# Kernel optimization log

Hardware: AMD Instinct MI355X
Metric: run time of the kernel (lower is better)

Reference implementation:

```python
import jax, jax.numpy as jnp
import numpy as np

EPS = 1e-5
NUM_HEADS = 4
KEY_DIM = 16
HEAD_DIM = 16


def qconv(x, w, b=None, stride=1, pad=0, groups=1):
    """Quaternion conv via Hamilton product. x:[B,C,4,H,W], w:[4,Cout,Cin/g,kh,kw]."""
    def cc(a, ww):
        return jax.lax.conv_general_dilated(
            a, ww, (stride, stride), [(pad, pad), (pad, pad)],
            feature_group_count=groups,
            dimension_numbers=('NCHW', 'OIHW', 'NCHW'))
    xr, xi, xj, xk = x[:, :, 0], x[:, :, 1], x[:, :, 2], x[:, :, 3]
    wr, wi, wj, wk = w[0], w[1], w[2], w[3]
    yr = cc(xr, wr) - cc(xi, wi) - cc(xj, wj) - cc(xk, wk)
    yi = cc(xr, wi) + cc(xi, wr) + cc(xj, wk) - cc(xk, wj)
    yj = cc(xr, wj) - cc(xi, wk) + cc(xj, wr) + cc(xk, wi)
    yk = cc(xr, wk) + cc(xi, wj) - cc(xj, wi) + cc(xk, wr)
    y = jnp.stack([yr, yi, yj, yk], axis=2)  # [B,Cout,4,H,W]
    if b is not None:
        y = y + b[None, :, :, None, None]
    return y


def iqbn(x, g, b):
    """Independent quaternion batch norm: per (channel, component) over (B,H,W)."""
    mean = x.mean(axis=(0, 3, 4), keepdims=True)
    var = x.var(axis=(0, 3, 4), keepdims=True)
    xhat = (x - mean) * jax.lax.rsqrt(var + EPS)
    return g[None, :, :, None, None] * xhat + b[None, :, :, None, None]


def qattention(x, qkv_w, qkv_b, proj_w, proj_b, pe_w, pe_b, ng, nb):
    B, C, Q, H, W = x.shape
    N = H * W
    qkv = qconv(x, qkv_w, qkv_b)                       # [B,h,4,H,W]
    qkv = qkv.reshape(B, NUM_HEADS, 2 * KEY_DIM + HEAD_DIM, Q, N)
    q = qkv[:, :, :KEY_DIM]                             # [B,nh,kd,4,N]
    k = qkv[:, :, KEY_DIM:2 * KEY_DIM]                  # [B,nh,kd,4,N]
    v = qkv[:, :, 2 * KEY_DIM:]                         # [B,nh,hd,4,N]
    scale = KEY_DIM ** (-0.5)
    attn = jnp.einsum('bhdqn,bhdqm->bhqnm', q, k) * scale   # [B,nh,4,N,N]
    attn = jax.nn.softmax(attn, axis=-1)
    o = jnp.einsum('bhqnm,bhdqm->bhdqn', attn, v)       # [B,nh,hd,4,N]
    o = o.reshape(B, C, Q, H, W)
    pe = qconv(o, pe_w, pe_b, stride=1, pad=1, groups=C // 4)
    o = o + pe
    o = qconv(o, proj_w, proj_b)
    return iqbn(o, ng, nb)


def setup_inputs() -> dict:
    key = jax.random.key(0)
    ks = jax.random.split(key, 16)
    c1, c2, c = 128, 128, 64
    h = c + 2 * NUM_HEADS * KEY_DIM  # 192
    s = 0.05
    x = jax.random.normal(ks[0], (4, c1, 4, 32, 32), dtype=jnp.float32)
    return {
        'x': x,
        'cv1_w': jax.random.normal(ks[1], (4, 2 * c, c1, 1, 1), jnp.float32) * s,
        'bn1_g': jnp.ones((2 * c, 4), jnp.float32),
        'bn1_b': jnp.zeros((2 * c, 4), jnp.float32),
        'qkv_w': jax.random.normal(ks[2], (4, h, c, 1, 1), jnp.float32) * s,
        'qkv_b': jnp.zeros((h, 4), jnp.float32),
        'proj_w': jax.random.normal(ks[3], (4, c, c, 1, 1), jnp.float32) * s,
        'proj_b': jnp.zeros((c, 4), jnp.float32),
        'pe_w': jax.random.normal(ks[4], (4, c, 4, 3, 3), jnp.float32) * s,  # groups=c//4=16
        'pe_b': jnp.zeros((c, 4), jnp.float32),
        'attn_norm_g': jnp.ones((c, 4), jnp.float32),
        'attn_norm_b': jnp.zeros((c, 4), jnp.float32),
        'ffn1_w': jax.random.normal(ks[5], (4, 2 * c, c, 1, 1), jnp.float32) * s,
        'ffn_bn1_g': jnp.ones((2 * c, 4), jnp.float32),
        'ffn_bn1_b': jnp.zeros((2 * c, 4), jnp.float32),
        'ffn2_w': jax.random.normal(ks[6], (4, c, 2 * c, 1, 1), jnp.float32) * s,
        'ffn_bn2_g': jnp.ones((c, 4), jnp.float32),
        'ffn_bn2_b': jnp.zeros((c, 4), jnp.float32),
        'cv2_w': jax.random.normal(ks[7], (4, c2, 2 * c, 1, 1), jnp.float32) * s,
        'bn2_g': jnp.ones((c2, 4), jnp.float32),
        'bn2_b': jnp.zeros((c2, 4), jnp.float32),
    }


def reference(x, cv1_w, bn1_g, bn1_b, qkv_w, qkv_b, proj_w, proj_b, pe_w, pe_b,
              attn_norm_g, attn_norm_b, ffn1_w, ffn_bn1_g, ffn_bn1_b,
              ffn2_w, ffn_bn2_g, ffn_bn2_b, cv2_w, bn2_g, bn2_b):
    h = jax.nn.relu(iqbn(qconv(x, cv1_w), bn1_g, bn1_b))  # [B,2c,4,H,W]
    c = h.shape[1] // 2
    a, b = h[:, :c], h[:, c:]
    a = qattention(a, qkv_w, qkv_b, proj_w, proj_b, pe_w, pe_b, attn_norm_g, attn_norm_b)
    a = jax.nn.relu(iqbn(qconv(a, ffn1_w), ffn_bn1_g, ffn_bn1_b))
    a = iqbn(qconv(a, ffn2_w), ffn_bn2_g, ffn_bn2_b)
    out = jnp.concatenate([a, b], axis=1)
    out = jax.nn.relu(iqbn(qconv(out, cv2_w), bn2_g, bn2_b))
    return out
```

## Files before the change

kernel.cpp:

```cpp
#include <hip/hip_runtime.h>

#define N_PIX 1024

typedef __attribute__((ext_vector_type(8))) short bf16x8;
typedef __attribute__((ext_vector_type(4))) float f32x4;

__device__ inline ushort f2bf(float f) {
    union { float f; unsigned u; } v; v.f = f;
    unsigned u = v.u;
    return (ushort)((u + 0x7FFF + ((u >> 16) & 1)) >> 16);
}
__device__ inline float bf2f(ushort h) {
    union { unsigned u; float f; } v; v.u = ((unsigned)h) << 16; return v.f;
}

__global__ __launch_bounds__(256) void wexpand_kernel(
    const float* __restrict__ w, ushort* __restrict__ wx, int Cout, int Cin)
{
    int idx = blockIdx.x * 256 + threadIdx.x;
    int K = 4 * Cin;
    if (idx >= 4 * Cout * K) return;
    int m = idx / K, k = idx - m * K;
    int co = m >> 2, c = m & 3, ci = k >> 2, cp = k & 3;
    const int   CT[4][4] = {{0,1,2,3},{1,0,3,2},{2,3,0,1},{3,2,1,0}};
    const float ST[4][4] = {{1.f,-1.f,-1.f,-1.f},{1.f,1.f,1.f,-1.f},
                            {1.f,-1.f,1.f,1.f},{1.f,1.f,-1.f,1.f}};
    float val = ST[c][cp] * w[(size_t)CT[c][cp] * Cout * Cin + (size_t)co * Cin + ci];
    wx[idx] = f2bf(val);
}

__global__ __launch_bounds__(256) void pack_kernel(
    const float* __restrict__ src, int sbs, ushort* __restrict__ xp, int K)
{
    __shared__ float t[32][257];
    const int k0 = blockIdx.x * 32;
    const int P0 = blockIdx.y * 256;
    const int b = P0 >> 10, p0 = P0 & 1023;
    const float* s = src + (size_t)b * sbs + (size_t)k0 * N_PIX + p0;
#pragma unroll
    for (int i = 0; i < 32; i++)
        t[i][threadIdx.x] = s[i * N_PIX + threadIdx.x];
    __syncthreads();
#pragma unroll
    for (int j = 0; j < 32; j++) {
        int flat = j * 256 + threadIdx.x;
        int kk = flat & 31, p = flat >> 5;
        xp[(size_t)(P0 + p) * K + k0 + kk] = f2bf(t[kk][p]);
    }
}

__global__ __launch_bounds__(256) void qgemm_kernel(
    const ushort* __restrict__ xp,
    const ushort* __restrict__ wx,
    const float* __restrict__ bias,
    float* __restrict__ y, int ybs,
    int M, int K)
{
    __shared__ ushort As[64 * 32];
    __shared__ ushort Bs[128 * 32];
    const int tid = threadIdx.x;
    const int m0 = blockIdx.x * 64;
    const int P0 = blockIdx.y * 128;
    const int b  = P0 >> 10;
    const int p0 = P0 & 1023;
    const int w  = tid >> 6;
    const int l  = tid & 63;
    const int wm = w >> 1, wn = w & 1;

    const f32x4 z = {0.f, 0.f, 0.f, 0.f};
    f32x4 acc[2][4];
#pragma unroll
    for (int mi = 0; mi < 2; mi++)
#pragma unroll
        for (int ni = 0; ni < 4; ni++) acc[mi][ni] = z;

    const int am  = tid >> 2, akb = tid & 3;
    const int lkb = l >> 4,   lr  = l & 15;

    for (int k0 = 0; k0 < K; k0 += 32) {
        __syncthreads();
        *(int4*)&As[((akb * 64) + am) * 8] =
            *(const int4*)&wx[(size_t)(m0 + am) * K + k0 + akb * 8];
#pragma unroll
        for (int it = 0; it < 2; it++) {
            int n = it * 64 + (tid >> 2);
            *(int4*)&Bs[((akb * 128) + n) * 8] =
                *(const int4*)&xp[(size_t)(P0 + n) * K + k0 + akb * 8];
        }
        __syncthreads();

        bf16x8 af[2], bf[4];
#pragma unroll
        for (int mi = 0; mi < 2; mi++)
            af[mi] = *(const bf16x8*)&As[((lkb * 64) + wm * 32 + mi * 16 + lr) * 8];
#pragma unroll
        for (int ni = 0; ni < 4; ni++)
            bf[ni] = *(const bf16x8*)&Bs[((lkb * 128) + wn * 64 + ni * 16 + lr) * 8];
#pragma unroll
        for (int mi = 0; mi < 2; mi++)
#pragma unroll
            for (int ni = 0; ni < 4; ni++)
                acc[mi][ni] = __builtin_amdgcn_mfma_f32_16x16x32_bf16(
                    af[mi], bf[ni], acc[mi][ni], 0, 0, 0);
    }

    float* yb = y + (size_t)b * ybs;
#pragma unroll
    for (int mi = 0; mi < 2; mi++) {
        int mrow = m0 + wm * 32 + mi * 16 + lkb * 4;
#pragma unroll
        for (int ni = 0; ni < 4; ni++) {
            int col = p0 + wn * 64 + ni * 16 + lr;
#pragma unroll
            for (int r = 0; r < 4; r++) {
                float v = acc[mi][ni][r];
                if (bias) v += bias[mrow + r];
                yb[(size_t)(mrow + r) * N_PIX + col] = v;
            }
        }
    }
}

__global__ __launch_bounds__(256) void iqbn_stats_kernel(
    const float* __restrict__ x, int xbs, float* __restrict__ stats)
{
    const int cq = blockIdx.x;
    float s = 0.f, s2 = 0.f;
#pragma unroll
    for (int b = 0; b < 4; b++) {
        const float* xp = x + (size_t)b * xbs + (size_t)cq * N_PIX;
        for (int p = threadIdx.x; p < N_PIX; p += 256) {
            float v = xp[p];
            s += v; s2 += v * v;
        }
    }
#pragma unroll
    for (int o = 32; o > 0; o >>= 1) {
        s  += __shfl_down(s, o);
        s2 += __shfl_down(s2, o);
    }
    __shared__ float red[8];
    int wid = threadIdx.x >> 6, lane = threadIdx.x & 63;
    if (lane == 0) { red[wid * 2] = s; red[wid * 2 + 1] = s2; }
    __syncthreads();
    if (threadIdx.x == 0) {
        s = 0.f; s2 = 0.f;
#pragma unroll
        for (int i = 0; i < 4; i++) { s += red[2 * i]; s2 += red[2 * i + 1]; }
        const float inv = 1.0f / 4096.0f;
        float mean = s * inv;
        float var  = s2 * inv - mean * mean;
        stats[cq * 2]     = mean;
        stats[cq * 2 + 1] = rsqrtf(var + 1e-5f);
    }
}

__global__ __launch_bounds__(256) void iqbn_apply_kernel(
    const float* __restrict__ x, int xbs,
    float* __restrict__ y, int ybs,
    const float* __restrict__ stats,
    const float* __restrict__ g, const float* __restrict__ bta,
    int C4, int relu)
{
    int cq = blockIdx.x % C4;
    int b  = blockIdx.x / C4;
    float mean = stats[cq * 2], rstd = stats[cq * 2 + 1];
    float ga = g[cq] * rstd;
    float bb = bta[cq] - mean * ga;
    const float4* xp = (const float4*)(x + (size_t)b * xbs + (size_t)cq * N_PIX);
    float4*       yp = (float4*)(y + (size_t)b * ybs + (size_t)cq * N_PIX);
    float4 v = xp[threadIdx.x];
    v.x = v.x * ga + bb; v.y = v.y * ga + bb; v.z = v.z * ga + bb; v.w = v.w * ga + bb;
    if (relu) {
        v.x = fmaxf(v.x, 0.f); v.y = fmaxf(v.y, 0.f);
        v.z = fmaxf(v.z, 0.f); v.w = fmaxf(v.w, 0.f);
    }
    yp[threadIdx.x] = v;
}

__global__ __launch_bounds__(256) void qattn_kernel(
    const float* __restrict__ qkv, float* __restrict__ o)
{
    __shared__ __attribute__((aligned(16))) char smem[24576];
    const int tid = threadIdx.x;
    const int grp = blockIdx.x;
    const int qc = grp & 3, hd = (grp >> 2) & 3, b = grp >> 4;
    const int n0 = blockIdx.y << 7;
    const int w = tid >> 6, lid = tid & 63;
    const int col = lid & 15, g = lid >> 4;
    const int swz = (col & 7) << 4;

    const float* gq = qkv + ((size_t)(b * 192 + hd * 48) * 4 + qc) * N_PIX;

    bf16x8 qf[2];
#pragma unroll
    for (int ns = 0; ns < 2; ns++) {
        int n = n0 + w * 32 + ns * 16 + col;
        const float* qg = gq + (size_t)((g & 1) * 8) * 4096 + n;
        union { bf16x8 v; ushort u[8]; } qq;
#pragma unroll
        for (int j = 0; j < 8; j++) {
            float qv = qg[(size_t)j * 4096] * 0.25f;
            ushort h = f2bf(qv);
            qq.u[j] = (g >= 2) ? f2bf(qv - bf2f(h)) : h;
        }
        qf[ns] = qq.v;
    }

    const f32x4 z = {0.f, 0.f, 0.f, 0.f};
    f32x4 O[2] = {z, z};
    float M[2] = {-1e30f, -1e30f}, L[2] = {0.f, 0.f};

    const int ml = tid & 63;
    const int d4 = (tid >> 6) << 2;

    for (int t = 0; t < 16; t++) {
        const int m0 = t << 6;
        __syncthreads();
        {
            const float* kg = gq + (size_t)(16 + d4) * 4096 + m0 + ml;
            const float* vg = gq + (size_t)(32 + d4) * 4096 + m0 + ml;
            float kv[4], vv[4];
#pragma unroll
            for (int i = 0; i < 4; i++) {
                kv[i] = kg[(size_t)i * 4096];
                vv[i] = vg[(size_t)i * 4096];
            }
            ushort kh[4], kl[4];
#pragma unroll
            for (int i = 0; i < 4; i++) {
                kh[i] = f2bf(kv[i]);
                kl[i] = f2bf(kv[i] - bf2f(kh[i]));
            }
            int sw = (ml & 7) << 4;
            int kbh = (ml * 64 + d4 * 2) ^ sw;
            int kbl = (ml * 64 + 32 + d4 * 2) ^ sw;
            *(uint2*)(smem + kbh) =
                make_uint2((uint)kh[0] | ((uint)kh[1] << 16), (uint)kh[2] | ((uint)kh[3] << 16));
            *(uint2*)(smem + kbl) =
                make_uint2((uint)kl[0] | ((uint)kl[1] << 16), (uint)kl[2] | ((uint)kl[3] << 16));
#pragma unroll
            for (int i = 0; i < 4; i++) {
                int d = d4 + i;
                ushort vh = f2bf(vv[i]);
                ushort vl = f2bf(vv[i] - bf2f(vh));
                int vb = (d * 128 + ml * 2) ^ ((d & 7) << 4);
                *(ushort*)(smem + 4096 + vb) = vh;
                *(ushort*)(smem + 6144 + vb) = vl;
            }
        }
        __syncthreads();

        f32x4 s[2][4];
#pragma unroll
        for (int ms = 0; ms < 4; ms++) {
            int rowb = (ms * 16 + col) * 64;
            bf16x8 a1 = *(const bf16x8*)(smem + ((rowb + g * 16) ^ swz));
            bf16x8 a2 = *(const bf16x8*)(smem + ((rowb + ((g ^ 2) * 16)) ^ swz));
#pragma unroll
            for (int ns = 0; ns < 2; ns++) {
                f32x4 c = __builtin_amdgcn_mfma_f32_16x16x32_bf16(a1, qf[ns], z, 0, 0, 0);
                s[ns][ms] = __builtin_amdgcn_mfma_f32_16x16x32_bf16(a2, qf[ns], c, 0, 0, 0);
            }
        }

#pragma unroll
        for (int ns = 0; ns < 2; ns++) {
            float tmax = s[ns][0][0];
#pragma unroll
            for (int ms = 0; ms < 4; ms++)
#pragma unroll
                for (int r = 0; r < 4; r++) tmax = fmaxf(tmax, s[ns][ms][r]);
            tmax = fmaxf(tmax, __shfl_xor(tmax, 16));
            tmax = fmaxf(tmax, __shfl_xor(tmax, 32));
            float Mn = fmaxf(M[ns], tmax);
            float rs = __expf(M[ns] - Mn);
            M[ns] = Mn;
            float psum = 0.f;
#pragma unroll
            for (int ms = 0; ms < 4; ms++) {
                f32x4 e;
#pragma unroll
                for (int r = 0; r < 4; r++) {
                    e[r] = __expf(s[ns][ms][r] - Mn);
                    psum += e[r];
                }
                s[ns][ms] = e;
            }
            psum += __shfl_xor(psum, 16);
            psum += __shfl_xor(psum, 32);
            L[ns] = L[ns] * rs + psum;
#pragma unroll
            for (int r = 0; r < 4; r++)
                O[ns][r] *= __shfl(rs, g * 4 + r);
            int nl = ns * 16 + col;
#pragma unroll
            for (int ms = 0; ms < 4; ms++) {
                uint plo = (uint)f2bf(s[ns][ms][0]) | ((uint)f2bf(s[ns][ms][1]) << 16);
                uint phi = (uint)f2bf(s[ns][ms][2]) | ((uint)f2bf(s[ns][ms][3]) << 16);
                int pb = (8192 + w * 4096 + nl * 128 + ms * 32 + g * 8) ^ swz;
                *(uint2*)(smem + pb) = make_uint2(plo, phi);
            }
        }
        __builtin_amdgcn_sched_barrier(0);

#pragma unroll
        for (int s2 = 0; s2 < 2; s2++) {
            int mb = s2 * 64 + g * 16;
            int vb = (col * 128 + mb) ^ swz;
            bf16x8 bvh = *(const bf16x8*)(smem + 4096 + vb);
            bf16x8 bvl = *(const bf16x8*)(smem + 6144 + vb);
#pragma unroll
            for (int ns = 0; ns < 2; ns++) {
                int nl = ns * 16 + col;
                bf16x8 ap = *(const bf16x8*)(smem + ((8192 + w * 4096 + nl * 128 + mb) ^ swz));
                O[ns] = __builtin_amdgcn_mfma_f32_16x16x32_bf16(ap, bvh, O[ns], 0, 0, 0);
                O[ns] = __builtin_amdgcn_mfma_f32_16x16x32_bf16(ap, bvl, O[ns], 0, 0, 0);
            }
        }
    }

#pragma unroll
    for (int ns = 0; ns < 2; ns++) {
        float invL = 1.f / L[ns];
#pragma unroll
        for (int r = 0; r < 4; r++)
            O[ns][r] *= __shfl(invL, g * 4 + r);
    }
    __syncthreads();
#pragma unroll
    for (int ns = 0; ns < 2; ns++) {
        int nloc = w * 32 + ns * 16 + g * 4;
        int ob = (8192 + col * 512 + nloc * 4) ^ swz;
        *(f32x4*)(smem + ob) = O[ns];
    }
    __syncthreads();
    {
        int d = tid >> 4, nb = (tid & 15) << 3;
        int b0 = (8192 + d * 512 + nb * 4) ^ ((d & 7) << 4);
        int b1 = (8192 + d * 512 + nb * 4 + 16) ^ ((d & 7) << 4);
        float4 o0 = *(const float4*)(smem + b0);
        float4 o1 = *(const float4*)(smem + b1);
        float* op = o + ((size_t)(b * 64 + hd * 16 + d) * 4 + qc) * N_PIX + n0 + nb;
        *(float4*)op = o0;
        *(float4*)(op + 4) = o1;
    }
}

__global__ __launch_bounds__(256) void pe_conv_kernel(
    const float* __restrict__ x,
    const float* __restrict__ w,
    const float* __restrict__ bias,
    float* __restrict__ y)
{
    const int bid = blockIdx.x;
    const int pt = bid & 3, co = (bid >> 2) & 63, b = bid >> 8;
    const int p = (pt << 8) + threadIdx.x;
    const int hh = p >> 5, ww = p & 31;
    const int g4 = (co >> 2) << 2;

    float a0 = bias[co * 4 + 0], a1 = bias[co * 4 + 1];
    float a2 = bias[co * 4 + 2], a3 = bias[co * 4 + 3];
    const float* xb = x + (size_t)b * 64 * 4096;
    const float* wb = w + co * 36;

#pragma unroll
    for (int dy = 0; dy < 3; dy++) {
        int yy = hh + dy - 1;
        if ((unsigned)yy >= 32u) continue;
#pragma unroll
        for (int dx = 0; dx < 3; dx++) {
            int xx = ww + dx - 1;
            if ((unsigned)xx >= 32u) continue;
            int sp = yy * 32 + xx;
#pragma unroll
            for (int cl = 0; cl < 4; cl++) {
                const float* xp = xb + (size_t)(g4 + cl) * 4096 + sp;
                float xr = xp[0], xi = xp[1024], xj = xp[2048], xk = xp[3072];
                const float* wp = wb + cl * 9 + dy * 3 + dx;
                float wr = wp[0], wi = wp[2304], wj2 = wp[4608], wk = wp[6912];
                a0 += xr * wr - xi * wi  - xj * wj2 - xk * wk;
                a1 += xr * wi + xi * wr  + xj * wk  - xk * wj2;
                a2 += xr * wj2 - xi * wk + xj * wr  + xk * wi;
                a3 += xr * wk + xi * wj2 - xj * wi  + xk * wr;
            }
        }
    }
    size_t ob = (size_t)b * 64 * 4096 + (size_t)co * 4096 + p;
    y[ob]        = x[ob]        + a0;
    y[ob + 1024] = x[ob + 1024] + a1;
    y[ob + 2048] = x[ob + 2048] + a2;
    y[ob + 3072] = x[ob + 3072] + a3;
}

extern "C" void kernel_launch(void* const* d_in, const int* in_sizes, int n_in,
                              void* d_out, int out_size, void* d_ws, size_t ws_size,
                              hipStream_t stream)
{
    const float* x      = (const float*)d_in[0];
    const float* cv1_w  = (const float*)d_in[1];
    const float* bn1_g  = (const float*)d_in[2];
    const float* bn1_b  = (const float*)d_in[3];
    const float* qkv_w  = (const float*)d_in[4];
    const float* qkv_b  = (const float*)d_in[5];
    const float* proj_w = (const float*)d_in[6];
    const float* proj_b = (const float*)d_in[7];
    const float* pe_w   = (const float*)d_in[8];
    const float* pe_b   = (const float*)d_in[9];
    const float* ang    = (const float*)d_in[10];
    const float* anb    = (const float*)d_in[11];
    const float* ffn1_w = (const float*)d_in[12];
    const float* fbn1_g = (const float*)d_in[13];
    const float* fbn1_b = (const float*)d_in[14];
    const float* ffn2_w = (const float*)d_in[15];
    const float* fbn2_g = (const float*)d_in[16];
    const float* fbn2_b = (const float*)d_in[17];
    const float* cv2_w  = (const float*)d_in[18];
    const float* bn2_g  = (const float*)d_in[19];
    const float* bn2_b  = (const float*)d_in[20];
    float* out = (float*)d_out;

    float* ws    = (float*)d_ws;
    float* hbuf  = ws;
    float* qkvb  = ws + 2097152;
    float* bufA  = ws + 5242880;
    float* bufD  = ws + 6291456;
    float* stats = ws + 8388608;
    ushort* Xp   = (ushort*)(ws + 8389632);
    ushort* Wx   = (ushort*)(ws + 9438208);
    float* bufB  = qkvb;
    float* bufC  = qkvb + 1048576;
    float* cv2o  = qkvb;

    const int S128 = 128 * 4096, S192 = 192 * 4096, S64 = 64 * 4096;

    wexpand_kernel<<<1024, 256, 0, stream>>>(cv1_w, Wx, 128, 128);
    pack_kernel<<<dim3(16, 16), 256, 0, stream>>>(x, S128, Xp, 512);
    qgemm_kernel<<<dim3(8, 32), 256, 0, stream>>>(Xp, Wx, nullptr, hbuf, S128, 512, 512);
    iqbn_stats_kernel<<<512, 256, 0, stream>>>(hbuf, S128, stats);
    iqbn_apply_kernel<<<2048, 256, 0, stream>>>(hbuf, S128, hbuf, S128, stats, bn1_g, bn1_b, 512, 1);

    wexpand_kernel<<<768, 256, 0, stream>>>(qkv_w, Wx, 192, 64);
    pack_kernel<<<dim3(8, 16), 256, 0, stream>>>(hbuf, S128, Xp, 256);
    qgemm_kernel<<<dim3(12, 32), 256, 0, stream>>>(Xp, Wx, qkv_b, qkvb, S192, 768, 256);

    qattn_kernel<<<dim3(64, 8), 256, 0, stream>>>(qkvb, bufA);

    pe_conv_kernel<<<1024, 256, 0, stream>>>(bufA, pe_w, pe_b, bufB);

    wexpand_kernel<<<256, 256, 0, stream>>>(proj_w, Wx, 64, 64);
    pack_kernel<<<dim3(8, 16), 256, 0, stream>>>(bufB, S64, Xp, 256);
    qgemm_kernel<<<dim3(4, 32), 256, 0, stream>>>(Xp, Wx, proj_b, bufC, S64, 256, 256);
    iqbn_stats_kernel<<<256, 256, 0, stream>>>(bufC, S64, stats);
    iqbn_apply_kernel<<<1024, 256, 0, stream>>>(bufC, S64, bufC, S64, stats, ang, anb, 256, 0);

    wexpand_kernel<<<512, 256, 0, stream>>>(ffn1_w, Wx, 128, 64);
    pack_kernel<<<dim3(8, 16), 256, 0, stream>>>(bufC, S64, Xp, 256);
    qgemm_kernel<<<dim3(8, 32), 256, 0, stream>>>(Xp, Wx, nullptr, bufD, S128, 512, 256);
    iqbn_stats_kernel<<<512, 256, 0, stream>>>(bufD, S128, stats);
    iqbn_apply_kernel<<<2048, 256, 0, stream>>>(bufD, S128, bufD, S128, stats, fbn1_g, fbn1_b, 512, 1);

    wexpand_kernel<<<512, 256, 0, stream>>>(ffn2_w, Wx, 64, 128);
    pack_kernel<<<dim3(16, 16), 256, 0, stream>>>(bufD, S128, Xp, 512);
    qgemm_kernel<<<dim3(4, 32), 256, 0, stream>>>(Xp, Wx, nullptr, bufA, S64, 256, 512);
    iqbn_stats_kernel<<<256, 256, 0, stream>>>(bufA, S64, stats);
    iqbn_apply_kernel<<<1024, 256, 0, stream>>>(bufA, S64, hbuf, S128, stats, fbn2_g, fbn2_b, 256, 0);

    wexpand_kernel<<<1024, 256, 0, stream>>>(cv2_w, Wx, 128, 128);
    pack_kernel<<<dim3(16, 16), 256, 0, stream>>>(hbuf, S128, Xp, 512);
    qgemm_kernel<<<dim3(8, 32), 256, 0, stream>>>(Xp, Wx, nullptr, cv2o, S128, 512, 512);
    iqbn_stats_kernel<<<512, 256, 0, stream>>>(cv2o, S128, stats);
    iqbn_apply_kernel<<<2048, 256, 0, stream>>>(cv2o, S128, out, S128, stats, bn2_g, bn2_b, 512, 1);
}
```

Measured before the change: 307.2 us.

## Fuse BN stats into GEMM epilogue and BN apply into bf16 packing

The new GEMM kernel uses a 64x64 tile with double-buffered LDS and register prefetch, and accumulates per-channel sum and sum-of-squares via shuffle reductions and atomics in its epilogue. This removes the separate stats pass. BN apply, ReLU and transpose-to-bf16 packing are fused into one kernel that writes straight into the next GEMM's packed input, including the concat split into the cv2 input buffer. This drops several full-tensor read/write passes and launches. In exchange it relies on float atomics, so stat accumulation order is nondeterministic, and variance is computed from raw sums.

After: 364.6 us. +18.7%, slower.

```diff
diff --git a/kernel.cpp b/kernel.cpp
--- a/kernel.cpp
+++ b/kernel.cpp
@@ -12,6 +12,12 @@
 }
 __device__ inline float bf2f(ushort h) {
     union { unsigned u; float f; } v; v.u = ((unsigned)h) << 16; return v.f;
+}
+
+__global__ __launch_bounds__(256) void zero_kernel(float* __restrict__ p, int n)
+{
+    int i = blockIdx.x * 256 + threadIdx.x;
+    if (i < n) p[i] = 0.f;
 }
 
 __global__ __launch_bounds__(256) void wexpand_kernel(
@@ -49,126 +55,60 @@
     }
 }
 
-__global__ __launch_bounds__(256) void qgemm_kernel(
-    const ushort* __restrict__ xp,
-    const ushort* __restrict__ wx,
-    const float* __restrict__ bias,
-    float* __restrict__ y, int ybs,
-    int M, int K)
-{
-    __shared__ ushort As[64 * 32];
-    __shared__ ushort Bs[128 * 32];
-    const int tid = threadIdx.x;
-    const int m0 = blockIdx.x * 64;
-    const int P0 = blockIdx.y * 128;
-    const int b  = P0 >> 10;
-    const int p0 = P0 & 1023;
-    const int w  = tid >> 6;
-    const int l  = tid & 63;
-    const int wm = w >> 1, wn = w & 1;
-
-    const f32x4 z = {0.f, 0.f, 0.f, 0.f};
-    f32x4 acc[2][4];
-#pragma unroll
-    for (int mi = 0; mi < 2; mi++)
-#pragma unroll
-        for (int ni = 0; ni < 4; ni++) acc[mi][ni] = z;
-
-    const int am  = tid >> 2, akb = tid & 3;
-    const int lkb = l >> 4,   lr  = l & 15;
-
-    for (int k0 = 0; k0 < K; k0 += 32) {
-        __syncthreads();
-        *(int4*)&As[((akb * 64) + am) * 8] =
-            *(const int4*)&wx[(size_t)(m0 + am) * K + k0 + akb * 8];
-#pragma unroll
-        for (int it = 0; it < 2; it++) {
-            int n = it * 64 + (tid >> 2);
-            *(int4*)&Bs[((akb * 128) + n) * 8] =
-                *(const int4*)&xp[(size_t)(P0 + n) * K + k0 + akb * 8];
-        }
-        __syncthreads();
-
-        bf16x8 af[2], bf[4];
-#pragma unroll
-        for (int mi = 0; mi < 2; mi++)
-            af[mi] = *(const bf16x8*)&As[((lkb * 64) + wm * 32 + mi * 16 + lr) * 8];
-#pragma unroll
-        for (int ni = 0; ni < 4; ni++)
-            bf[ni] = *(const bf16x8*)&Bs[((lkb * 128) + wn * 64 + ni * 16 + lr) * 8];
-#pragma unroll
-        for (int mi = 0; mi < 2; mi++)
-#pragma unroll
-            for (int ni = 0; ni < 4; ni++)
-                acc[mi][ni] = __builtin_amdgcn_mfma_f32_16x16x32_bf16(
-                    af[mi], bf[ni], acc[mi][ni], 0, 0, 0);
-    }
-
-    float* yb = y + (size_t)b * ybs;
-#pragma unroll
-    for (int mi = 0; mi < 2; mi++) {
-        int mrow = m0 + wm * 32 + mi * 16 + lkb * 4;
-#pragma unroll
-        for (int ni = 0; ni < 4; ni++) {
-            int col = p0 + wn * 64 + ni * 16 + lr;
-#pragma unroll
-            for (int r = 0; r < 4; r++) {
-                float v = acc[mi][ni][r];
-                if (bias) v += bias[mrow + r];
-                yb[(size_t)(mrow + r) * N_PIX + col] = v;
-            }
-        }
-    }
-}
-
-__global__ __launch_bounds__(256) void iqbn_stats_kernel(
-    const float* __restrict__ x, int xbs, float* __restrict__ stats)
-{
-    const int cq = blockIdx.x;
-    float s = 0.f, s2 = 0.f;
-#pragma unroll
-    for (int b = 0; b < 4; b++) {
-        const float* xp = x + (size_t)b * xbs + (size_t)cq * N_PIX;
-        for (int p = threadIdx.x; p < N_PIX; p += 256) {
-            float v = xp[p];
-            s += v; s2 += v * v;
-        }
-    }
-#pragma unroll
-    for (int o = 32; o > 0; o >>= 1) {
-        s  += __shfl_down(s, o);
-        s2 += __shfl_down(s2, o);
-    }
-    __shared__ float red[8];
-    int wid = threadIdx.x >> 6, lane = threadIdx.x & 63;
-    if (lane == 0) { red[wid * 2] = s; red[wid * 2 + 1] = s2; }
+__global__ __launch_bounds__(256) void applypack_kernel(
+    const float* __restrict__ y, int M,
+    const float* __restrict__ sraw,
+    const float* __restrict__ g, const float* __restrict__ bta,
+    ushort* __restrict__ dst0, int ld0,
+    ushort* __restrict__ dst1, int ld1, int ksplit, int relu)
+{
+    __shared__ float t[32][257];
+    __shared__ float gs[32], bs[32];
+    const int k0 = blockIdx.x * 32;
+    const int P0 = blockIdx.y * 256;
+    const int b = P0 >> 10, p0 = P0 & 1023;
+    if (threadIdx.x < 32) {
+        int k = k0 + threadIdx.x;
+        float mean = sraw[k * 2] * (1.f / 4096.f);
+        float var  = sraw[k * 2 + 1] * (1.f / 4096.f) - mean * mean;
+        float rs = rsqrtf(var + 1e-5f);
+        float gg = g[k] * rs;
+        gs[threadIdx.x] = gg;
+        bs[threadIdx.x] = bta[k] - mean * gg;
+    }
     __syncthreads();
-    if (threadIdx.x == 0) {
-        s = 0.f; s2 = 0.f;
-#pragma unroll
-        for (int i = 0; i < 4; i++) { s += red[2 * i]; s2 += red[2 * i + 1]; }
-        const float inv = 1.0f / 4096.0f;
-        float mean = s * inv;
-        float var  = s2 * inv - mean * mean;
-        stats[cq * 2]     = mean;
-        stats[cq * 2 + 1] = rsqrtf(var + 1e-5f);
-    }
-}
-
-__global__ __launch_bounds__(256) void iqbn_apply_kernel(
-    const float* __restrict__ x, int xbs,
-    float* __restrict__ y, int ybs,
-    const float* __restrict__ stats,
-    const float* __restrict__ g, const float* __restrict__ bta,
-    int C4, int relu)
-{
-    int cq = blockIdx.x % C4;
-    int b  = blockIdx.x / C4;
-    float mean = stats[cq * 2], rstd = stats[cq * 2 + 1];
-    float ga = g[cq] * rstd;
+    const float* s = y + (size_t)b * M * N_PIX + (size_t)k0 * N_PIX + p0;
+#pragma unroll
+    for (int i = 0; i < 32; i++) {
+        float v = s[i * N_PIX + threadIdx.x] * gs[i] + bs[i];
+        if (relu) v = fmaxf(v, 0.f);
+        t[i][threadIdx.x] = v;
+    }
+    __syncthreads();
+#pragma unroll
+    for (int j = 0; j < 32; j++) {
+        int flat = j * 256 + threadIdx.x;
+        int kk = flat & 31, p = flat >> 5;
+        int k = k0 + kk;
+        ushort h = f2bf(t[kk][p]);
+        if (k < ksplit) dst0[(size_t)(P0 + p) * ld0 + k] = h;
+        else            dst1[(size_t)(P0 + p) * ld1 + k] = h;
+    }
+}
+
+__global__ __launch_bounds__(256) void iqbn_apply2_kernel(
+    const float* __restrict__ x, float* __restrict__ y,
+    const float* __restrict__ sraw,
+    const float* __restrict__ g, const float* __restrict__ bta, int relu)
+{
+    int cq = blockIdx.x & 511, b = blockIdx.x >> 9;
+    float mean = sraw[cq * 2] * (1.f / 4096.f);
+    float var  = sraw[cq * 2 + 1] * (1.f / 4096.f) - mean * mean;
+    float rs = rsqrtf(var + 1e-5f);
+    float ga = g[cq] * rs;
     float bb = bta[cq] - mean * ga;
-    const float4* xp = (const float4*)(x + (size_t)b * xbs + (size_t)cq * N_PIX);
-    float4*       yp = (float4*)(y + (size_t)b * ybs + (size_t)cq * N_PIX);
+    const float4* xp = (const float4*)(x + ((size_t)b * 512 + cq) * N_PIX);
+    float4*       yp = (float4*)(y + ((size_t)b * 512 + cq) * N_PIX);
     float4 v = xp[threadIdx.x];
     v.x = v.x * ga + bb; v.y = v.y * ga + bb; v.z = v.z * ga + bb; v.w = v.w * ga + bb;
     if (relu) {
@@ -176,6 +116,118 @@
         v.z = fmaxf(v.z, 0.f); v.w = fmaxf(v.w, 0.f);
     }
     yp[threadIdx.x] = v;
+}
+
+__global__ __launch_bounds__(256) void qgemm2_kernel(
+    const ushort* __restrict__ xp,
+    const ushort* __restrict__ wx,
+    const float* __restrict__ bias,
+    float* __restrict__ y,
+    float* __restrict__ sraw,
+    int M, int K)
+{
+    __shared__ ushort As[2][8 * 64 * 8];
+    __shared__ ushort Bs[2][8 * 64 * 8];
+    const int tid = threadIdx.x;
+    const int m0 = blockIdx.x * 64;
+    const int n0 = blockIdx.y * 64;
+    const int w = tid >> 6, l = tid & 63;
+    const int wm = w >> 1, wn = w & 1;
+    const int lr = l & 15, lkb = l >> 4;
+    const int srow = tid >> 2, sk8 = tid & 3;
+
+    const ushort* ga = wx + (size_t)(m0 + srow) * K + sk8 * 8;
+    const ushort* gb = xp + (size_t)(n0 + srow) * K + sk8 * 8;
+
+    int4 ra0, ra1, rb0, rb1;
+#define LOADT(T) { int ko = (T) << 6; \
+    ra0 = *(const int4*)(ga + ko);      ra1 = *(const int4*)(ga + ko + 32); \
+    rb0 = *(const int4*)(gb + ko);      rb1 = *(const int4*)(gb + ko + 32); }
+#define WRITET(BUF) { \
+    *(int4*)&As[BUF][((sk8    ) * 64 + srow) * 8] = ra0; \
+    *(int4*)&As[BUF][((sk8 + 4) * 64 + srow) * 8] = ra1; \
+    *(int4*)&Bs[BUF][((sk8    ) * 64 + srow) * 8] = rb0; \
+    *(int4*)&Bs[BUF][((sk8 + 4) * 64 + srow) * 8] = rb1; }
+
+    const f32x4 z = {0.f, 0.f, 0.f, 0.f};
+    f32x4 acc[2][2] = {{z, z}, {z, z}};
+    const int nt = K >> 6;
+
+    LOADT(0);
+    WRITET(0);
+    __syncthreads();
+
+    for (int t = 0; t < nt; ++t) {
+        if (t + 1 < nt) LOADT(t + 1);
+        const int bsel = t & 1;
+#pragma unroll
+        for (int kk = 0; kk < 2; kk++) {
+            bf16x8 af[2], bf[2];
+#pragma unroll
+            for (int mi = 0; mi < 2; mi++)
+                af[mi] = *(const bf16x8*)&As[bsel][((kk * 4 + lkb) * 64 + wm * 32 + mi * 16 + lr) * 8];
+#pragma unroll
+            for (int ni = 0; ni < 2; ni++)
+                bf[ni] = *(const bf16x8*)&Bs[bsel][((kk * 4 + lkb) * 64 + wn * 32 + ni * 16 + lr) * 8];
+#pragma unroll
+            for (int mi = 0; mi < 2; mi++)
+#pragma unroll
+                for (int ni = 0; ni < 2; ni++)
+                    acc[mi][ni] = __builtin_amdgcn_mfma_f32_16x16x32_bf16(
+                        af[mi], bf[ni], acc[mi][ni], 0, 0, 0);
+        }
+        __syncthreads();
+        if (t + 1 < nt) WRITET((t + 1) & 1);
+        __syncthreads();
+    }
+#undef LOADT
+#undef WRITET
+
+    if (bias) {
+#pragma unroll
+        for (int mi = 0; mi < 2; mi++)
+#pragma unroll
+            for (int r = 0; r < 4; r++) {
+                float bv = bias[m0 + wm * 32 + mi * 16 + lkb * 4 + r];
+#pragma unroll
+                for (int ni = 0; ni < 2; ni++) acc[mi][ni][r] += bv;
+            }
+    }
+
+#pragma unroll
+    for (int mi = 0; mi < 2; mi++) {
+        int mrow = m0 + wm * 32 + mi * 16 + lkb * 4;
+#pragma unroll
+        for (int ni = 0; ni < 2; ni++) {
+            int col = n0 + wn * 32 + ni * 16 + lr;
+            int bb = col >> 10, p = col & 1023;
+            float* yb = y + (size_t)bb * M * N_PIX + (size_t)mrow * N_PIX + p;
+#pragma unroll
+            for (int r = 0; r < 4; r++) yb[(size_t)r * N_PIX] = acc[mi][ni][r];
+        }
+    }
+
+    if (sraw) {
+#pragma unroll
+        for (int mi = 0; mi < 2; mi++) {
+#pragma unroll
+            for (int r = 0; r < 4; r++) {
+                float a0 = acc[mi][0][r], a1 = acc[mi][1][r];
+                float sv = a0 + a1;
+                float s2 = a0 * a0 + a1 * a1;
+#pragma unroll
+                for (int o = 1; o < 16; o <<= 1) {
+                    sv += __shfl_xor(sv, o);
+                    s2 += __shfl_xor(s2, o);
+                }
+                if (lr == 0) {
+                    int row = m0 + wm * 32 + mi * 16 + lkb * 4 + r;
+                    atomicAdd(&sraw[row * 2], sv);
+                    atomicAdd(&sraw[row * 2 + 1], s2);
+                }
+            }
+        }
+    }
 }
 
 __global__ __launch_bounds__(256) void qattn_kernel(
@@ -420,55 +472,61 @@
     const float* bn2_b  = (const float*)d_in[20];
     float* out = (float*)d_out;
 
-    float* ws    = (float*)d_ws;
-    float* hbuf  = ws;
-    float* qkvb  = ws + 2097152;
-    float* bufA  = ws + 5242880;
-    float* bufD  = ws + 6291456;
-    float* stats = ws + 8388608;
-    ushort* Xp   = (ushort*)(ws + 8389632);
-    ushort* Wx   = (ushort*)(ws + 9438208);
-    float* bufB  = qkvb;
-    float* bufC  = qkvb + 1048576;
-    float* cv2o  = qkvb;
-
-    const int S128 = 128 * 4096, S192 = 192 * 4096, S64 = 64 * 4096;
+    float* ws = (float*)d_ws;
+    float*  qkvb  = ws;
+    float*  bufA  = ws + 3145728;
+    float*  rawA  = ws + 4194304;
+    float*  rawB  = ws + 6291456;
+    float*  stats = ws + 7340032;
+    ushort* Wx    = (ushort*)(ws + 7350272);
+    ushort* XpIn  = (ushort*)(ws + 7481344);
+    ushort* XpA   = (ushort*)(ws + 8529920);
+    ushort* XpCv2 = (ushort*)(ws + 9054208);
+    float*  bufB  = qkvb;
+    ushort* XpF1  = XpIn;
+    ushort* XpF2  = XpIn;
+    ushort* XpP   = XpA;
+
+    float* st_cv1  = stats;
+    float* st_proj = stats + 2048;
+    float* st_ffn1 = stats + 4096;
+    float* st_ffn2 = stats + 6144;
+    float* st_cv2  = stats + 8192;
+
+    const int S128 = 128 * 4096, S64 = 64 * 4096;
+
+    zero_kernel<<<40, 256, 0, stream>>>(stats, 10240);
 
     wexpand_kernel<<<1024, 256, 0, stream>>>(cv1_w, Wx, 128, 128);
-    pack_kernel<<<dim3(16, 16), 256, 0, stream>>>(x, S128, Xp, 512);
-    qgemm_kernel<<<dim3(8, 32), 256, 0, stream>>>(Xp, Wx, nullptr, hbuf, S128, 512, 512);
-    iqbn_stats_kernel<<<512, 256, 0, stream>>>(hbuf, S128, stats);
-    iqbn_apply_kernel<<<2048, 256, 0, stream>>>(hbuf, S128, hbuf, S128, stats, bn1_g, bn1_b, 512, 1);
+    pack_kernel<<<dim3(16, 16), 256, 0, stream>>>(x, S128, XpIn, 512);
+    qgemm2_kernel<<<dim3(8, 64), 256, 0, stream>>>(XpIn, Wx, nullptr, rawA, st_cv1, 512, 512);
+    applypack_kernel<<<dim3(16, 16), 256, 0, stream>>>(rawA, 512, st_cv1, bn1_g, bn1_b,
+                                                       XpA, 256, XpCv2, 512, 256, 1);
 
     wexpand_kernel<<<768, 256, 0, stream>>>(qkv_w, Wx, 192, 64);
-    pack_kernel<<<dim3(8, 16), 256, 0, stream>>>(hbuf, S128, Xp, 256);
-    qgemm_kernel<<<dim3(12, 32), 256, 0, stream>>>(Xp, Wx, qkv_b, qkvb, S192, 768, 256);
+    qgemm2_kernel<<<dim3(12, 64), 256, 0, stream>>>(XpA, Wx, qkv_b, qkvb, nullptr, 768, 256);
 
     qattn_kernel<<<dim3(64, 8), 256, 0, stream>>>(qkvb, bufA);
 
     pe_conv_kernel<<<1024, 256, 0, stream>>>(bufA, pe_w, pe_b, bufB);
+    pack_kernel<<<dim3(8, 16), 256, 0, stream>>>(bufB, S64, XpP, 256);
 
     wexpand_kernel<<<256, 256, 0, stream>>>(proj_w, Wx, 64, 64);
-    pack_kernel<<<dim3(8, 16), 256, 0, stream>>>(bufB, S64, Xp, 256);
-    qgemm_kernel<<<dim3(4, 32), 256, 0, stream>>>(Xp, Wx, proj_b, bufC, S64, 256, 256);
-    iqbn_stats_kernel<<<256, 256, 0, stream>>>(bufC, S64, stats);
-    iqbn_apply_kernel<<<1024, 256, 0, stream>>>(bufC, S64, bufC, S64, stats, ang, anb, 256, 0);
+    qgemm2_kernel<<<dim3(4, 64), 256, 0, stream>>>(XpP, Wx, proj_b, rawB, st_proj, 256, 256);
+    applypack_kernel<<<dim3(8, 16), 256, 0, stream>>>(rawB, 256, st_proj, ang, anb,
+                                                      XpF1, 256, XpF1, 256, 1 << 20, 0);
 
     wexpand_kernel<<<512, 256, 0, stream>>>(ffn1_w, Wx, 128, 64);
-    pack_kernel<<<dim3(8, 16), 256, 0, stream>>>(bufC, S64, Xp, 256);
-    qgemm_kernel<<<dim3(8, 32), 256, 0, stream>>>(Xp, Wx, nullptr, bufD, S128, 512, 256);
-    iqbn_stats_kernel<<<512, 256, 0, stream>>>(bufD, S128, stats);
-    iqbn_apply_kernel<<<2048, 256, 0, stream>>>(bufD, S128, bufD, S128, stats, fbn1_g, fbn1_b, 512, 1);
+    qgemm2_kernel<<<dim3(8, 64), 256, 0, stream>>>(XpF1, Wx, nullptr, rawA, st_ffn1, 512, 256);
+    applypack_kernel<<<dim3(16, 16), 256, 0, stream>>>(rawA, 512, st_ffn1, fbn1_g, fbn1_b,
+                                                       XpF2, 512, XpF2, 512, 1 << 20, 1);
 
     wexpand_kernel<<<512, 256, 0, stream>>>(ffn2_w, Wx, 64, 128);
-    pack_kernel<<<dim3(16, 16), 256, 0, stream>>>(bufD, S128, Xp, 512);
-    qgemm_kernel<<<dim3(4, 32), 256, 0, stream>>>(Xp, Wx, nullptr, bufA, S64, 256, 512);
-    iqbn_stats_kernel<<<256, 256, 0, stream>>>(bufA, S64, stats);
-    iqbn_apply_kernel<<<1024, 256, 0, stream>>>(bufA, S64, hbuf, S128, stats, fbn2_g, fbn2_b, 256, 0);
+    qgemm2_kernel<<<dim3(4, 64), 256, 0, stream>>>(XpF2, Wx, nullptr, rawB, st_ffn2, 256, 512);
+    applypack_kernel<<<dim3(8, 16), 256, 0, stream>>>(rawB, 256, st_ffn2, fbn2_g, fbn2_b,
+                                                      XpCv2, 512, XpCv2, 512, 1 << 20, 0);
 
     wexpand_kernel<<<1024, 256, 0, stream>>>(cv2_w, Wx, 128, 128);
-    pack_kernel<<<dim3(16, 16), 256, 0, stream>>>(hbuf, S128, Xp, 512);
-    qgemm_kernel<<<dim3(8, 32), 256, 0, stream>>>(Xp, Wx, nullptr, cv2o, S128, 512, 512);
-    iqbn_stats_kernel<<<512, 256, 0, stream>>>(cv2o, S128, stats);
-    iqbn_apply_kernel<<<2048, 256, 0, stream>>>(cv2o, S128, out, S128, stats, bn2_g, bn2_b, 512, 1);
-}
+    qgemm2_kernel<<<dim3(8, 64), 256, 0, stream>>>(XpCv2, Wx, nullptr, rawA, st_cv2, 512, 512);
+    iqbn_apply2_kernel<<<2048, 256, 0, stream>>>(rawA, out, st_cv2, bn2_g, bn2_b, 1);
+}
```
